# Kernel tuning notes

Hardware: AMD Instinct MI355X
Metric: run time of the kernel (lower is better)

Reference implementation:

```python
import jax, jax.numpy as jnp
import numpy as np

B, S, HID = 1, 2048, 2048
NH, NKV, HD = 32, 8, 64
N_REP = NH // NKV
SCALE = HD ** -0.5
NEG = -1e9  # large negative for causal mask (finite to stay fp16-safe-ish)


def _rope_tables(seq_len, head_dim, base=10000.0):
    inv_freq = 1.0 / (base ** (np.arange(0, head_dim, 2, dtype=np.float32) / head_dim))
    t = np.arange(seq_len, dtype=np.float32)
    freqs = np.outer(t, inv_freq)                      # [S, HD/2]
    emb = np.concatenate([freqs, freqs], axis=-1)      # [S, HD]
    return jnp.asarray(np.cos(emb))[None], jnp.asarray(np.sin(emb))[None]  # [1,S,HD]


def setup_inputs() -> dict:
    key = jax.random.key(0)
    k1, k2, k3, k4, k5 = jax.random.split(key, 5)
    hidden_states = jax.random.normal(k1, (B, S, HID), dtype=jnp.float32)
    cos, sin = _rope_tables(S, HD)
    # causal additive mask [1,1,S,S]
    causal = jnp.tril(jnp.ones((S, S), dtype=bool))
    attention_mask = jnp.where(causal, 0.0, NEG).astype(jnp.float32)[None, None]
    init = 0.02
    wq = jax.random.normal(k2, (NH * HD, HID), dtype=jnp.float32) * init
    wk = jax.random.normal(k3, (NKV * HD, HID), dtype=jnp.float32) * init
    wv = jax.random.normal(k4, (NKV * HD, HID), dtype=jnp.float32) * init
    wo = jax.random.normal(k5, (HID, NH * HD), dtype=jnp.float32) * init
    return {"hidden_states": hidden_states, "cos": cos, "sin": sin,
            "attention_mask": attention_mask, "wq": wq, "wk": wk, "wv": wv, "wo": wo}


def _rotate_half(x):
    x1, x2 = jnp.split(x, 2, axis=-1)
    return jnp.concatenate([-x2, x1], axis=-1)


def reference(hidden_states, cos, sin, attention_mask, wq, wk, wv, wo):
    b, s, _ = hidden_states.shape
    q = (hidden_states @ wq.T).reshape(b, s, NH, HD).transpose(0, 2, 1, 3)   # [b,nh,s,hd]
    k = (hidden_states @ wk.T).reshape(b, s, NKV, HD).transpose(0, 2, 1, 3)  # [b,nkv,s,hd]
    v = (hidden_states @ wv.T).reshape(b, s, NKV, HD).transpose(0, 2, 1, 3)
    c = cos[:, None]  # [b,1,s,hd]
    sn = sin[:, None]
    q = q * c + _rotate_half(q) * sn
    k = k * c + _rotate_half(k) * sn
    # GQA repeat_kv
    k = jnp.repeat(k, N_REP, axis=1)  # [b,nh,s,hd]
    v = jnp.repeat(v, N_REP, axis=1)
    scores = jnp.einsum('bhqd,bhkd->bhqk', q, k) * SCALE
    scores = scores.astype(jnp.float32) + attention_mask
    probs = jax.nn.softmax(scores, axis=-1).astype(q.dtype)  # dropout p=0 (eval)
    attn = jnp.einsum('bhqk,bhkd->bhqd', probs, v)
    attn = attn.transpose(0, 2, 1, 3).reshape(b, s, NH * HD)
    return attn @ wo.T
```

## Files before the change

kernel.cpp:

```cpp
#include <hip/hip_runtime.h>
#include <hip/hip_bf16.h>
#include <stdint.h>


#define S_LEN 2048
#define HIDDEN 2048
#define NH 32
#define NKV 8
#define HD 64
#define SCALE_L2E 0.18033688011112042f

typedef __bf16 bf16x8 __attribute__((ext_vector_type(8)));
typedef float f32x4 __attribute__((ext_vector_type(4)));
typedef float f32x16 __attribute__((ext_vector_type(16)));

__device__ inline void gload16(const void* g, void* l) {
    using GP = const __attribute__((address_space(1))) uint32_t*;
    using LP = __attribute__((address_space(3))) uint32_t*;
    __builtin_amdgcn_global_load_lds((GP)g, (LP)(uint32_t)(uintptr_t)l, 16, 0, 0);
}

__device__ inline ushort bf16r(float x) {
    uint32_t u = __float_as_uint(x);
    return (ushort)((u + 0x7FFFu + ((u >> 16) & 1u)) >> 16);
}
__device__ inline void bsplit(float x, ushort& h, ushort& l) {
    uint32_t u = __float_as_uint(x);
    uint32_t hr = (u + 0x7FFFu + ((u >> 16) & 1u)) >> 16;
    float r = x - __uint_as_float(hr << 16);
    uint32_t ul = __float_as_uint(r);
    l = (ushort)((ul + 0x7FFFu + ((ul >> 16) & 1u)) >> 16);
    h = (ushort)hr;
}
__device__ inline uint32_t pk2(float a, float b) {
    return (uint32_t)bf16r(a) | ((uint32_t)bf16r(b) << 16);
}

__global__ __launch_bounds__(256) void split_bf16(
    const float* __restrict__ src, ushort* __restrict__ hi,
    ushort* __restrict__ lo, int n4)
{
    int i = blockIdx.x * 256 + threadIdx.x;
    if (i >= n4) return;
    float4 v = ((const float4*)src)[i];
    float x[4] = {v.x, v.y, v.z, v.w};
    ushort h[4], l[4];
#pragma unroll
    for (int j = 0; j < 4; j++) bsplit(x[j], h[j], l[j]);
    ushort4 ho = {h[0], h[1], h[2], h[3]};
    ushort4 lv = {l[0], l[1], l[2], l[3]};
    ((ushort4*)hi)[i] = ho;
    ((ushort4*)lo)[i] = lv;
}

__device__ inline int swz_idx(int row, int fk) {
    int line = row >> 1;
    int inner = (((fk << 1) | (row & 1)) ^ (line & 7));
    return line * 64 + inner * 8;
}

template <int MODE>
__global__ __launch_bounds__(256) void mfma_gemm(
    const ushort* __restrict__ Ah, const ushort* __restrict__ Al,
    const ushort* __restrict__ Bh, const ushort* __restrict__ Bl,
    float* __restrict__ C0, float* __restrict__ C1, float* __restrict__ C2,
    int ldc, int nbx)
{
    __shared__ ushort sAh[64 * 32], sAl[64 * 32];
    __shared__ ushort sBh[128 * 32], sBl[128 * 32];

    const int t = threadIdx.x;
    const int per = (int)gridDim.x >> 3;
    const int id = (blockIdx.x & 7) * per + (blockIdx.x >> 3);
    const int m0 = (id % nbx) * 64;
    const int n0 = (id / nbx) * 128;

    const int lineA = t >> 3;
    const int uA = (t & 7) ^ (lineA & 7);
    const int rowA = lineA * 2 + (uA & 1);
    const int kA = (uA >> 1) * 8;
    const ushort* aH = Ah + (size_t)(m0 + rowA) * HIDDEN + kA;
    const ushort* aL = Al + (size_t)(m0 + rowA) * HIDDEN + kA;
    const ushort* bH0 = Bh + (size_t)(n0 + rowA) * HIDDEN + kA;
    const ushort* bH1 = Bh + (size_t)(n0 + 64 + rowA) * HIDDEN + kA;
    const ushort* bL0 = Bl + (size_t)(n0 + rowA) * HIDDEN + kA;
    const ushort* bL1 = Bl + (size_t)(n0 + 64 + rowA) * HIDDEN + kA;

    const int lane = t & 63, w = t >> 6;
    const int fr = lane & 15;
    const int fk = lane >> 4;

    int idxA[4], idxB[2];
#pragma unroll
    for (int fi = 0; fi < 4; fi++) idxA[fi] = swz_idx(fi * 16 + fr, fk);
#pragma unroll
    for (int fj = 0; fj < 2; fj++) idxB[fj] = swz_idx(w * 32 + fj * 16 + fr, fk);

    f32x4 acc[4][2];
#pragma unroll
    for (int i = 0; i < 4; i++)
#pragma unroll
        for (int j = 0; j < 2; j++) acc[i][j] = {0.f, 0.f, 0.f, 0.f};

    for (int k0 = 0; k0 < HIDDEN; k0 += 32) {
        __syncthreads();
        gload16(aH + k0, sAh + t * 8);
        gload16(aL + k0, sAl + t * 8);
        gload16(bH0 + k0, sBh + t * 8);
        gload16(bH1 + k0, sBh + 2048 + t * 8);
        gload16(bL0 + k0, sBl + t * 8);
        gload16(bL1 + k0, sBl + 2048 + t * 8);
        __syncthreads();

        bf16x8 ah[4], al[4], bh[2], bl[2];
#pragma unroll
        for (int fi = 0; fi < 4; fi++) {
            ah[fi] = *(const bf16x8*)&sAh[idxA[fi]];
            al[fi] = *(const bf16x8*)&sAl[idxA[fi]];
        }
#pragma unroll
        for (int fj = 0; fj < 2; fj++) {
            bh[fj] = *(const bf16x8*)&sBh[idxB[fj]];
            bl[fj] = *(const bf16x8*)&sBl[idxB[fj]];
        }
#pragma unroll
        for (int fi = 0; fi < 4; fi++)
#pragma unroll
            for (int fj = 0; fj < 2; fj++) {
                acc[fi][fj] = __builtin_amdgcn_mfma_f32_16x16x32_bf16(
                    ah[fi], bh[fj], acc[fi][fj], 0, 0, 0);
                acc[fi][fj] = __builtin_amdgcn_mfma_f32_16x16x32_bf16(
                    ah[fi], bl[fj], acc[fi][fj], 0, 0, 0);
                acc[fi][fj] = __builtin_amdgcn_mfma_f32_16x16x32_bf16(
                    al[fi], bh[fj], acc[fi][fj], 0, 0, 0);
            }
    }

#pragma unroll
    for (int fi = 0; fi < 4; fi++)
#pragma unroll
        for (int fj = 0; fj < 2; fj++) {
            int row0 = m0 + fi * 16 + fk * 4;
            int gcol = n0 + w * 32 + fj * 16 + fr;
            if (MODE == 0) {
                int slot = gcol >> 6, cin = gcol & 63;
                float* dst;
                if (slot < NH) dst = C0 + (size_t)slot * S_LEN * HD;
                else if (slot < NH + NKV) dst = C1 + (size_t)(slot - NH) * S_LEN * HD;
                else dst = C2 + (size_t)(slot - NH - NKV) * S_LEN * HD;
#pragma unroll
                for (int i = 0; i < 4; i++)
                    dst[(size_t)(row0 + i) * HD + cin] = acc[fi][fj][i];
            } else {
#pragma unroll
                for (int i = 0; i < 4; i++)
                    C0[(size_t)(row0 + i) * ldc + gcol] = acc[fi][fj][i];
            }
        }
}

__global__ __launch_bounds__(256) void rope_split(
    float* __restrict__ qd, const float* __restrict__ kd,
    const float* __restrict__ cosT, const float* __restrict__ sinT,
    ushort* __restrict__ khi, ushort* __restrict__ klo)
{
    int idx = blockIdx.x * 256 + threadIdx.x;
    int d = idx & 31;
    int s = (idx >> 5) & (S_LEN - 1);
    int slot = idx >> 16;
    float c = cosT[s * HD + d];
    float sn = sinT[s * HD + d];
    if (slot < NH) {
        float* base = qd + ((size_t)slot * S_LEN + s) * HD;
        float x1 = base[d], x2 = base[d + 32];
        base[d] = x1 * c - x2 * sn;
        base[d + 32] = x2 * c + x1 * sn;
    } else {
        const float* base = kd + ((size_t)(slot - NH) * S_LEN + s) * HD;
        float x1 = base[d], x2 = base[d + 32];
        float y1 = x1 * c - x2 * sn;
        float y2 = x2 * c + x1 * sn;
        int sw = (s & 7) << 3;
        size_t rb = ((size_t)(slot - NH) * S_LEN + s) * 64;
        ushort h1, l1, h2, l2;
        bsplit(y1, h1, l1);
        bsplit(y2, h2, l2);
        khi[rb + (d ^ sw)] = h1;        klo[rb + (d ^ sw)] = l1;
        khi[rb + ((d + 32) ^ sw)] = h2; klo[rb + ((d + 32) ^ sw)] = l2;
    }
}

__global__ __launch_bounds__(256) void split_vt(
    const float* __restrict__ v, ushort* __restrict__ vthi,
    ushort* __restrict__ vtlo)
{
    __shared__ float tile[64][65];
    const int b = blockIdx.x;
    const int hk = b >> 5, kt = b & 31;
    const float* src = v + ((size_t)hk * S_LEN + kt * 64) * 64;
    const int t = threadIdx.x;
    {
        int row = t >> 2, dg = (t & 3) * 16;
#pragma unroll
        for (int i = 0; i < 4; i++) {
            float4 x = *(const float4*)(src + row * 64 + dg + i * 4);
            tile[row][dg + i * 4 + 0] = x.x;
            tile[row][dg + i * 4 + 1] = x.y;
            tile[row][dg + i * 4 + 2] = x.z;
            tile[row][dg + i * 4 + 3] = x.w;
        }
    }
    __syncthreads();
    const int d = t >> 2, kg = (t & 3) * 16;
    ushort hi16[16], lo16[16];
#pragma unroll
    for (int i = 0; i < 16; i++) bsplit(tile[kg + i][d], hi16[i], lo16[i]);
    const int sw = (d & 7) << 3;
    size_t rowb = ((size_t)hk * 64 + d) * S_LEN + kt * 64;
    int base = kg ^ (sw & 48);
    int o0 = base + (sw & 8);
    int o1 = base + (8 ^ (sw & 8));
    *(ushort4*)&vthi[rowb + o0]     = *(ushort4*)&hi16[0];
    *(ushort4*)&vthi[rowb + o0 + 4] = *(ushort4*)&hi16[4];
    *(ushort4*)&vthi[rowb + o1]     = *(ushort4*)&hi16[8];
    *(ushort4*)&vthi[rowb + o1 + 4] = *(ushort4*)&hi16[12];
    *(ushort4*)&vtlo[rowb + o0]     = *(ushort4*)&lo16[0];
    *(ushort4*)&vtlo[rowb + o0 + 4] = *(ushort4*)&lo16[4];
    *(ushort4*)&vtlo[rowb + o1]     = *(ushort4*)&lo16[8];
    *(ushort4*)&vtlo[rowb + o1 + 4] = *(ushort4*)&lo16[12];
}

__global__ __launch_bounds__(256, 2) void attn_mfma(
    const float* __restrict__ q,
    const ushort* __restrict__ khi, const ushort* __restrict__ klo,
    const ushort* __restrict__ vthi, const ushort* __restrict__ vtlo,
    ushort* __restrict__ oH, ushort* __restrict__ oL)
{
    __shared__ ushort uni[2][16384];
    __shared__ float corrw[4][32];
    __shared__ float lw[4][32];

    const int t = threadIdx.x;
    const int lane = t & 63, w = t >> 6;
    const int hi = lane >> 5;
    const int l31 = lane & 31;
    const int dh = hi * 8;

    const int id = blockIdx.x;
    const int hd_ = id & 31;
    const int g = id >> 5;
    const int qt = (g < 8) ? (15 - g) : (g - 8);
    const int q0 = qt * 128;
    const int hk = hd_ >> 2;

    const ushort* khi_t = khi + (size_t)hk * S_LEN * 64;
    const ushort* klo_t = klo + (size_t)hk * S_LEN * 64;
    const ushort* vth_t = vthi + (size_t)hk * 64 * S_LEN;
    const ushort* vtl_t = vtlo + (size_t)hk * 64 * S_LEN;
    const int d0s = t >> 3, kks = (t & 7) * 8;
    const int swk = (l31 & 7) << 3;
    const int qg = q0 + w * 32 + l31;
    const int ntiles = 2 * qt + 2;

    auto MF = [](bf16x8 a, bf16x8 b, f32x16 c) {
        return __builtin_amdgcn_mfma_f32_32x32x16_bf16(a, b, c, 0, 0, 0);
    };
    auto STAGE = [&](int k0, ushort* buf) {
        const ushort* a = khi_t + (size_t)k0 * 64;
        const ushort* b = klo_t + (size_t)k0 * 64;
        gload16(a + t * 8, buf + t * 8);
        gload16(a + 2048 + t * 8, buf + 2048 + t * 8);
        gload16(b + t * 8, buf + 4096 + t * 8);
        gload16(b + 2048 + t * 8, buf + 6144 + t * 8);
        gload16(vth_t + (size_t)d0s * S_LEN + k0 + kks, buf + 8192 + t * 8);
        gload16(vth_t + (size_t)(d0s + 32) * S_LEN + k0 + kks, buf + 10240 + t * 8);
        gload16(vtl_t + (size_t)d0s * S_LEN + k0 + kks, buf + 12288 + t * 8);
        gload16(vtl_t + (size_t)(d0s + 32) * S_LEN + k0 + kks, buf + 14336 + t * 8);
    };

    STAGE(0, uni[0]);
    {
        const int row = t >> 1, dg = (t & 1) * 32;
        const float* src = q + ((size_t)hd_ * S_LEN + q0 + row) * HD + dg;
        const int sw = (row & 7) << 3;
#pragma unroll
        for (int i = 0; i < 8; i++) {
            float4 v4 = *(const float4*)(src + i * 4);
            float xs[4] = {v4.x, v4.y, v4.z, v4.w};
            ushort h4[4], l4[4];
#pragma unroll
            for (int j = 0; j < 4; j++) bsplit(xs[j] * SCALE_L2E, h4[j], l4[j]);
            int idx = (row * 64 + dg + i * 4) ^ sw;
            *(ushort4*)&uni[1][idx] = *(ushort4*)&h4[0];
            *(ushort4*)&uni[1][8192 + idx] = *(ushort4*)&l4[0];
        }
    }
    __syncthreads();
    bf16x8 qh[4], ql[4];
    {
        const int qrow = w * 32 + l31;
        const int sw = (qrow & 7) << 3;
#pragma unroll
        for (int ks = 0; ks < 4; ks++) {
            int idx = (qrow * 64 + ks * 16 + dh) ^ sw;
            qh[ks] = *(const bf16x8*)&uni[1][idx];
            ql[ks] = *(const bf16x8*)&uni[1][8192 + idx];
        }
    }
    __syncthreads();

    f32x16 accO0, accO1;
#pragma unroll
    for (int r = 0; r < 16; r++) { accO0[r] = 0.f; accO1[r] = 0.f; }
    float m_run = -1e30f, l_run = 0.f;

    for (int tile = 0; tile < ntiles; tile++) {
        const int k0 = tile * 64;
        const ushort* U = uni[tile & 1];
        if (tile + 1 < ntiles) {
            STAGE(k0 + 64, uni[(tile + 1) & 1]);
            asm volatile("s_waitcnt vmcnt(8)" ::: "memory");
        } else {
            asm volatile("s_waitcnt vmcnt(0)" ::: "memory");
        }
        __builtin_amdgcn_s_barrier();

        f32x16 sa0, sa1, sb0, sb1;
#pragma unroll
        for (int r = 0; r < 16; r++) { sa0[r] = 0.f; sa1[r] = 0.f; sb0[r] = 0.f; sb1[r] = 0.f; }
        __builtin_amdgcn_s_setprio(1);
#pragma unroll
        for (int ks = 0; ks < 2; ks++) {
            int off = ks * 16 + dh;
            int i0 = (l31 * 64 + off) ^ swk;
            int i1 = ((l31 + 32) * 64 + off) ^ swk;
            bf16x8 kh0 = *(const bf16x8*)&U[i0];
            bf16x8 kl0 = *(const bf16x8*)&U[4096 + i0];
            bf16x8 kh1 = *(const bf16x8*)&U[i1];
            bf16x8 kl1 = *(const bf16x8*)&U[4096 + i1];
            sa0 = MF(kh0, qh[ks], sa0); sa1 = MF(kh1, qh[ks], sa1);
            sa0 = MF(kh0, ql[ks], sa0); sa1 = MF(kh1, ql[ks], sa1);
            sa0 = MF(kl0, qh[ks], sa0); sa1 = MF(kl1, qh[ks], sa1);
        }
#pragma unroll
        for (int ks = 2; ks < 4; ks++) {
            int off = ks * 16 + dh;
            int i0 = (l31 * 64 + off) ^ swk;
            int i1 = ((l31 + 32) * 64 + off) ^ swk;
            bf16x8 kh0 = *(const bf16x8*)&U[i0];
            bf16x8 kl0 = *(const bf16x8*)&U[4096 + i0];
            bf16x8 kh1 = *(const bf16x8*)&U[i1];
            bf16x8 kl1 = *(const bf16x8*)&U[4096 + i1];
            sb0 = MF(kh0, qh[ks], sb0); sb1 = MF(kh1, qh[ks], sb1);
            sb0 = MF(kh0, ql[ks], sb0); sb1 = MF(kh1, ql[ks], sb1);
            sb0 = MF(kl0, qh[ks], sb0); sb1 = MF(kl1, qh[ks], sb1);
        }
        __builtin_amdgcn_s_setprio(0);
        f32x16 sc0 = sa0 + sb0;
        f32x16 sc1 = sa1 + sb1;

        if (tile >= 2 * qt) {
#pragma unroll
            for (int r = 0; r < 16; r++) {
                int krow = (r & 3) + 8 * (r >> 2) + 4 * hi;
                if (k0 + krow > qg) sc0[r] = -1e30f;
                if (k0 + 32 + krow > qg) sc1[r] = -1e30f;
            }
        }
        float mx = -1e30f;
#pragma unroll
        for (int r = 0; r < 16; r++) mx = fmaxf(mx, fmaxf(sc0[r], sc1[r]));
        mx = fmaxf(mx, __shfl_xor(mx, 32));

        const bool skip = __all(mx - m_run <= 8.0f);
        float corr = 1.f;
        if (!skip) {
            float m_new = fmaxf(m_run, mx);
            corr = exp2f(m_run - m_new);
            m_run = m_new;
            if (lane < 32) corrw[w][l31] = corr;
        }
        float sum = 0.f;
#pragma unroll
        for (int r = 0; r < 16; r++) {
            float p0 = exp2f(sc0[r] - m_run);
            float p1 = exp2f(sc1[r] - m_run);
            sc0[r] = p0; sc1[r] = p1;
            sum += p0 + p1;
        }
        sum += __shfl_xor(sum, 32);
        l_run = l_run * corr + sum;

        bf16x8 pa[4];
        {
            uint32_t c0, c1, c2, c3;
            union { uint32_t u[4]; bf16x8 v; } uu;
#define BUILD_PA(SC, RB, DST)                                              \
            c0 = pk2((SC)[RB + 0], (SC)[RB + 1]);                          \
            c1 = pk2((SC)[RB + 2], (SC)[RB + 3]);                          \
            c2 = pk2((SC)[RB + 4], (SC)[RB + 5]);                          \
            c3 = pk2((SC)[RB + 6], (SC)[RB + 7]);                          \
            asm volatile("v_permlane32_swap_b32 %0, %1"                    \
                         : "+v"(c0), "+v"(c2));                            \
            asm volatile("v_permlane32_swap_b32 %0, %1"                    \
                         : "+v"(c1), "+v"(c3));                            \
            uu.u[0] = c0; uu.u[1] = c1; uu.u[2] = c2; uu.u[3] = c3;        \
            DST = uu.v;
            BUILD_PA(sc0, 0, pa[0]);
            BUILD_PA(sc0, 8, pa[1]);
            BUILD_PA(sc1, 0, pa[2]);
            BUILD_PA(sc1, 8, pa[3]);
#undef BUILD_PA
        }

        if (!skip) {
#pragma unroll
            for (int r = 0; r < 16; r++) {
                int qrow = (r & 3) + 8 * (r >> 2) + 4 * hi;
                float cr = corrw[w][qrow];
                accO0[r] *= cr; accO1[r] *= cr;
            }
        }

        __builtin_amdgcn_s_setprio(1);
#pragma unroll
        for (int ks = 0; ks < 4; ks++) {
            int off = ks * 16 + dh;
            int ia = (l31 * 64 + off) ^ swk;
            int ib = ((l31 + 32) * 64 + off) ^ swk;
            bf16x8 vh0 = *(const bf16x8*)&U[8192 + ia];
            bf16x8 vh1 = *(const bf16x8*)&U[8192 + ib];
            bf16x8 vl0 = *(const bf16x8*)&U[12288 + ia];
            bf16x8 vl1 = *(const bf16x8*)&U[12288 + ib];
            accO0 = MF(pa[ks], vh0, accO0);
            accO1 = MF(pa[ks], vh1, accO1);
            accO0 = MF(pa[ks], vl0, accO0);
            accO1 = MF(pa[ks], vl1, accO1);
        }
        __builtin_amdgcn_s_setprio(0);

        asm volatile("" ::: "memory");
        __builtin_amdgcn_s_barrier();
    }

    if (lane < 32) lw[w][l31] = l_run;
#pragma unroll
    for (int r = 0; r < 16; r++) {
        int qrow = (r & 3) + 8 * (r >> 2) + 4 * hi;
        float inv = 1.0f / lw[w][qrow];
        float v0 = accO0[r] * inv;
        float v1 = accO1[r] * inv;
        size_t base = (size_t)(q0 + w * 32 + qrow) * (NH * HD) + hd_ * 64 + l31;
        ushort hh, ll;
        bsplit(v0, hh, ll);
        oH[base] = hh; oL[base] = ll;
        bsplit(v1, hh, ll);
        oH[base + 32] = hh; oL[base + 32] = ll;
    }
}

extern "C" void kernel_launch(void* const* d_in, const int* in_sizes, int n_in,
                              void* d_out, int out_size, void* d_ws, size_t ws_size,
                              hipStream_t stream) {
    const float* hidden = (const float*)d_in[0];
    const float* cosT   = (const float*)d_in[1];
    const float* sinT   = (const float*)d_in[2];
    const float* wq = (const float*)d_in[4];
    const float* wk = (const float*)d_in[5];
    const float* wv = (const float*)d_in[6];
    const float* wo = (const float*)d_in[7];
    float* out = (float*)d_out;

    char* wsb = (char*)d_ws;
    auto alloc = [&](size_t bytes) { char* p = wsb; wsb += (bytes + 255) & ~255ULL; return p; };
    float* q = (float*)alloc((size_t)NH * S_LEN * HD * 4);
    float* k = (float*)alloc((size_t)NKV * S_LEN * HD * 4);
    float* v = (float*)alloc((size_t)NKV * S_LEN * HD * 4);
    ushort* hidH = (ushort*)alloc((size_t)S_LEN * HIDDEN * 2);
    ushort* hidL = (ushort*)alloc((size_t)S_LEN * HIDDEN * 2);
    ushort* WcH  = (ushort*)alloc((size_t)3072 * HIDDEN * 2);
    ushort* WcL  = (ushort*)alloc((size_t)3072 * HIDDEN * 2);
    ushort* woH  = (ushort*)alloc((size_t)HIDDEN * 2048 * 2);
    ushort* woL  = (ushort*)alloc((size_t)HIDDEN * 2048 * 2);
    ushort* oH   = (ushort*)alloc((size_t)S_LEN * 2048 * 2);
    ushort* oL   = (ushort*)alloc((size_t)S_LEN * 2048 * 2);
    ushort* khi  = hidH;
    ushort* klo  = hidH + 1048576;
    ushort* vthi = hidH + 2097152;
    ushort* vtlo = hidH + 3145728;

    dim3 blk(256);
    {
        int n4 = S_LEN * HIDDEN / 4;
        split_bf16<<<(n4 + 255) / 256, blk, 0, stream>>>(hidden, hidH, hidL, n4);
        int nq4 = NH * HD * HIDDEN / 4;
        split_bf16<<<(nq4 + 255) / 256, blk, 0, stream>>>(wq, WcH, WcL, nq4);
        int nk4 = NKV * HD * HIDDEN / 4;
        size_t off = (size_t)NH * HD * HIDDEN;
        split_bf16<<<(nk4 + 255) / 256, blk, 0, stream>>>(wk, WcH + off, WcL + off, nk4);
        size_t off2 = off + (size_t)NKV * HD * HIDDEN;
        split_bf16<<<(nk4 + 255) / 256, blk, 0, stream>>>(wv, WcH + off2, WcL + off2, nk4);
        int nw4 = HIDDEN * 2048 / 4;
        split_bf16<<<(nw4 + 255) / 256, blk, 0, stream>>>(wo, woH, woL, nw4);
    }
    mfma_gemm<0><<<dim3(32 * 24), blk, 0, stream>>>(
        hidH, hidL, WcH, WcL, q, k, v, 0, 32);
    rope_split<<<(NH + NKV) * S_LEN * 32 / 256, blk, 0, stream>>>(
        q, k, cosT, sinT, khi, klo);
    split_vt<<<NKV * (S_LEN / 64), blk, 0, stream>>>(v, vthi, vtlo);
    attn_mfma<<<dim3(512), blk, 0, stream>>>(
        q, khi, klo, vthi, vtlo, oH, oL);
    mfma_gemm<1><<<dim3(32 * 16), blk, 0, stream>>>(
        oH, oL, woH, woL, out, nullptr, nullptr, 2048, 32);
}
```

Before: 385.9 us.

## Double-buffer LDS tiles in split-bf16 MFMA GEMM to overlap loads with compute

Gives the A and B shared-memory tiles of the GEMM kernel two buffers each. The global-to-LDS loads for the next K step are issued before the MFMAs of the current step, and a partial vmcnt wait plus raw s_barrier replaces the two __syncthreads per iteration. The aim is to hide global load latency behind the matrix math. In exchange it doubles LDS use, which can lower occupancy, and it depends on the hand-written vmcnt counts being correct.

```diff
diff --git a/kernel.cpp b/kernel.cpp
--- a/kernel.cpp
+++ b/kernel.cpp
@@ -66,8 +66,8 @@
     float* __restrict__ C0, float* __restrict__ C1, float* __restrict__ C2,
     int ldc, int nbx)
 {
-    __shared__ ushort sAh[64 * 32], sAl[64 * 32];
-    __shared__ ushort sBh[128 * 32], sBl[128 * 32];
+    __shared__ ushort sAh[2][64 * 32], sAl[2][64 * 32];
+    __shared__ ushort sBh[2][128 * 32], sBl[2][128 * 32];
 
     const int t = threadIdx.x;
     const int per = (int)gridDim.x >> 3;
@@ -102,26 +102,37 @@
 #pragma unroll
         for (int j = 0; j < 2; j++) acc[i][j] = {0.f, 0.f, 0.f, 0.f};
 
-    for (int k0 = 0; k0 < HIDDEN; k0 += 32) {
-        __syncthreads();
-        gload16(aH + k0, sAh + t * 8);
-        gload16(aL + k0, sAl + t * 8);
-        gload16(bH0 + k0, sBh + t * 8);
-        gload16(bH1 + k0, sBh + 2048 + t * 8);
-        gload16(bL0 + k0, sBl + t * 8);
-        gload16(bL1 + k0, sBl + 2048 + t * 8);
-        __syncthreads();
+    auto STAGE = [&](int k0, int b) {
+        gload16(aH + k0, sAh[b] + t * 8);
+        gload16(aL + k0, sAl[b] + t * 8);
+        gload16(bH0 + k0, sBh[b] + t * 8);
+        gload16(bH1 + k0, sBh[b] + 2048 + t * 8);
+        gload16(bL0 + k0, sBl[b] + t * 8);
+        gload16(bL1 + k0, sBl[b] + 2048 + t * 8);
+    };
+
+    STAGE(0, 0);
+    const int NSTEP = HIDDEN / 32;
+    for (int i = 0; i < NSTEP; i++) {
+        const int cur = i & 1;
+        if (i + 1 < NSTEP) {
+            STAGE((i + 1) * 32, cur ^ 1);
+            asm volatile("s_waitcnt vmcnt(6)" ::: "memory");
+        } else {
+            asm volatile("s_waitcnt vmcnt(0)" ::: "memory");
+        }
+        __builtin_amdgcn_s_barrier();
 
         bf16x8 ah[4], al[4], bh[2], bl[2];
 #pragma unroll
         for (int fi = 0; fi < 4; fi++) {
-            ah[fi] = *(const bf16x8*)&sAh[idxA[fi]];
-            al[fi] = *(const bf16x8*)&sAl[idxA[fi]];
+            ah[fi] = *(const bf16x8*)&sAh[cur][idxA[fi]];
+            al[fi] = *(const bf16x8*)&sAl[cur][idxA[fi]];
         }
 #pragma unroll
         for (int fj = 0; fj < 2; fj++) {
-            bh[fj] = *(const bf16x8*)&sBh[idxB[fj]];
-            bl[fj] = *(const bf16x8*)&sBl[idxB[fj]];
+            bh[fj] = *(const bf16x8*)&sBh[cur][idxB[fj]];
+            bl[fj] = *(const bf16x8*)&sBl[cur][idxB[fj]];
         }
 #pragma unroll
         for (int fi = 0; fi < 4; fi++)
@@ -134,6 +145,7 @@
                 acc[fi][fj] = __builtin_amdgcn_mfma_f32_16x16x32_bf16(
                     al[fi], bh[fj], acc[fi][fj], 0, 0, 0);
             }
+        __builtin_amdgcn_s_barrier();
     }
 
 #pragma unroll
```

After: 381.5 us. About the same (-1.2%).
